# Kernel optimization log

Hardware: AMD Instinct MI355X
Metric: run time of the kernel (lower is better)

Reference implementation:

```python
import jax, jax.numpy as jnp
import numpy as np

K = 3      # spline order
NUM = 5    # grid intervals


def bspline_basis(x, grid, k=K):
    """Cox-de Boor recursion. x: (B, D); grid: (num+2k+1,) extended knots.
    Returns basis of shape (B, D, num+k)."""
    xe = x[..., None]                                       # (B, D, 1)
    B = ((xe >= grid[:-1]) & (xe < grid[1:])).astype(x.dtype)  # (B, D, num+2k)
    for p in range(1, k + 1):
        left = (xe - grid[:-(p + 1)]) / (grid[p:-1] - grid[:-(p + 1)])
        right = (grid[p + 1:] - xe) / (grid[p + 1:] - grid[1:-p])
        B = left * B[..., :-1] + right * B[..., 1:]
    return B                                                # (B, D, num+k)


def kan_layer(x, grid, coef, sb, sp, mask, bias):
    """phi(x)[b,o] = sum_i mask[o,i]*(sb[o,i]*silu(x[b,i]) + sp[o,i]*sum_c B[b,i,c]*coef[o,i,c]) + bias[o]"""
    Bsp = bspline_basis(x, grid)                            # (B, in, C)
    spline = jnp.einsum('bic,oic->bo', Bsp, coef * (sp * mask)[:, :, None])
    base = jnp.einsum('bi,oi->bo', jax.nn.silu(x), sb * mask)
    return base + spline + bias


def setup_inputs() -> dict:
    key = jax.random.key(0)
    ks = jax.random.split(key, 6)
    Bch, d0, d1, d2 = 8192, 1024, 2048, 1024
    C = NUM + K                                 # 8 spline coeffs per edge
    h = 2.0 / NUM                               # grid_range [-1,1]
    # extended knot vector: k extra knots each side, num+2k+1 = 12 points
    grid = jnp.arange(-K, NUM + K + 1, dtype=jnp.float32) * h - 1.0
    return {
        "x": jax.random.normal(ks[0], (Bch, d0), jnp.float32) * 0.5,
        "coef0": jax.random.normal(ks[1], (d1, d0, C), jnp.float32) * 0.1,
        "sb0": jax.random.normal(ks[2], (d1, d0), jnp.float32) / np.sqrt(d0).astype(np.float32),
        "sp0": jnp.ones((d1, d0), jnp.float32),
        "mask0": jnp.ones((d1, d0), jnp.float32),
        "bias0": jnp.zeros((d1,), jnp.float32),
        "coef1": jax.random.normal(ks[3], (d2, d1, C), jnp.float32) * 0.1,
        "sb1": jax.random.normal(ks[4], (d2, d1), jnp.float32) / np.sqrt(d1).astype(np.float32),
        "sp1": jnp.ones((d2, d1), jnp.float32),
        "mask1": jnp.ones((d2, d1), jnp.float32),
        "bias1": jnp.zeros((d2,), jnp.float32),
        "grid": grid,
    }


def reference(x, coef0, sb0, sp0, mask0, bias0, coef1, sb1, sp1, mask1, bias1, grid):
    h1 = kan_layer(x, grid, coef0, sb0, sp0, mask0, bias0)
    out = kan_layer(h1, grid, coef1, sb1, sp1, mask1, bias1)
    return out
```

## Files before the change

### kernel.cpp

```cpp
#include <hip/hip_runtime.h>
#include <hip/hip_bf16.h>
#include <cstdint>


typedef __attribute__((ext_vector_type(8))) short short8;
typedef __attribute__((ext_vector_type(4))) short short4v;
typedef __attribute__((ext_vector_type(4))) float f32x4;

#define GLD16(gp, lp)                                                          \
  __builtin_amdgcn_global_load_lds(                                           \
      (const __attribute__((address_space(1))) unsigned int*)(gp),             \
      (__attribute__((address_space(3))) unsigned int*)(lp), 16, 0, 0)

__device__ __forceinline__ unsigned short f2bf(float f) {
  __hip_bfloat16 h = __float2bfloat16(f);
  return *reinterpret_cast<unsigned short*>(&h);
}

__device__ __forceinline__ void basis8(float x, float* w, int& j) {
  float u  = (x + 2.2f) * 2.5f;
  float fj = floorf(u);
  j = (int)fj;
  float t  = u - fj;
  float omt = 1.0f - t;
  float t2 = t * t, t3 = t2 * t;
  w[0] = omt * omt * omt * (1.0f / 6.0f);
  w[1] = (3.0f * t3 - 6.0f * t2 + 4.0f) * (1.0f / 6.0f);
  w[2] = (-3.0f * t3 + 3.0f * t2 + 3.0f * t + 1.0f) * (1.0f / 6.0f);
  w[3] = t3 * (1.0f / 6.0f);
}

__device__ __forceinline__ void prep_w_item(
    long idx, const float* __restrict__ coef, const float* __restrict__ sb,
    const float* __restrict__ sp, const float* __restrict__ mask,
    __hip_bfloat16* __restrict__ W, int I) {
  int qtr = I >> 2;
  int iq = (int)(idx % qtr);
  int o  = (int)(idx / qtr);
  int i  = iq << 2;
  size_t oi = (size_t)o * I + i;
  float4 mk4 = *(const float4*)(mask + oi);
  float4 sp4 = *(const float4*)(sp + oi);
  float4 sb4 = *(const float4*)(sb + oi);
  float spm[4] = {sp4.x * mk4.x, sp4.y * mk4.y, sp4.z * mk4.z, sp4.w * mk4.w};
  float cf[4][8];
  const float4* cp = (const float4*)(coef + oi * 8);
#pragma unroll
  for (int e = 0; e < 4; e++) {
    float4 a = cp[e * 2], b = cp[e * 2 + 1];
    cf[e][0] = a.x; cf[e][1] = a.y; cf[e][2] = a.z; cf[e][3] = a.w;
    cf[e][4] = b.x; cf[e][5] = b.y; cf[e][6] = b.z; cf[e][7] = b.w;
  }
  __hip_bfloat16* base = W + (size_t)o * (size_t)(9 * I) + (i >> 6) * 576 + (i & 63);
#pragma unroll
  for (int c = 0; c < 8; c++) {
    short4v pk;
#pragma unroll
    for (int e = 0; e < 4; e++) pk[e] = (short)f2bf(cf[e][c] * spm[e]);
    *(short4v*)(base + c * 64) = pk;
  }
  short4v ps;
  ps[0] = (short)f2bf(sb4.x * mk4.x); ps[1] = (short)f2bf(sb4.y * mk4.y);
  ps[2] = (short)f2bf(sb4.z * mk4.z); ps[3] = (short)f2bf(sb4.w * mk4.w);
  *(short4v*)(base + 8 * 64) = ps;
}

__device__ __forceinline__ void expand_item(
    long idx, const float* __restrict__ src, __hip_bfloat16* __restrict__ aug,
    int I) {
  int  oct = I >> 3;
  int  io = (int)(idx % oct);
  long b  = idx / oct;
  int  i  = io << 3;
  const float* sp = src + b * (size_t)I + i;
  float4 xa = *(const float4*)sp;
  float4 xb = *(const float4*)(sp + 4);
  float xv[8] = {xa.x, xa.y, xa.z, xa.w, xb.x, xb.y, xb.z, xb.w};

  float w[8][4], s[8];
  int   j[8];
#pragma unroll
  for (int e = 0; e < 8; e++) {
    float xe = xv[e];
    s[e] = xe / (1.0f + __expf(-xe));
    basis8(xe, w[e], j[e]);
  }
  __hip_bfloat16* base = aug + b * (size_t)(9 * I) + (i >> 6) * 576 + (i & 63);
#pragma unroll
  for (int c = 0; c < 8; c++) {
    short8 pk;
#pragma unroll
    for (int e = 0; e < 8; e++) {
      int d = j[e] - c;
      float v = 0.0f;
      v = (d == 0) ? w[e][3] : v;
      v = (d == 1) ? w[e][2] : v;
      v = (d == 2) ? w[e][1] : v;
      v = (d == 3) ? w[e][0] : v;
      pk[e] = (short)f2bf(v);
    }
    *(short8*)(base + c * 64) = pk;
  }
  short8 ps;
#pragma unroll
  for (int e = 0; e < 8; e++) ps[e] = (short)f2bf(s[e]);
  *(short8*)(base + 8 * 64) = ps;
}

__global__ void prep_merge(
    const float* __restrict__ coef, const float* __restrict__ sb,
    const float* __restrict__ sp, const float* __restrict__ mask,
    __hip_bfloat16* __restrict__ W, int IW, long nW,
    const float* __restrict__ xsrc, __hip_bfloat16* __restrict__ aug,
    int IX, long nX) {
  long idx = (long)blockIdx.x * blockDim.x + threadIdx.x;
  if (idx < nW)            prep_w_item(idx, coef, sb, sp, mask, W, IW);
  else if (idx < nW + nX)  expand_item(idx - nW, xsrc, aug, IX);
}

__global__ void expand_aug(const float* __restrict__ src,
                           __hip_bfloat16* __restrict__ aug,
                           long totalOcts, int I) {
  long idx = (long)blockIdx.x * blockDim.x + threadIdx.x;
  if (idx >= totalOcts) return;
  expand_item(idx, src, aug, I);
}

template <int BN>
__global__ __launch_bounds__(512, 4) void gemm128(
    const __hip_bfloat16* __restrict__ A, const __hip_bfloat16* __restrict__ Bw,
    const float* __restrict__ bias, float* __restrict__ Cout, int N, int K) {
  constexpr int WN   = BN / 4;
  constexpr int NREP = BN / 64;
  constexpr int BUFB = 8192 + BN * 64;
  __shared__ __attribute__((aligned(16))) char lds[3 * BUFB];

  const int t = threadIdx.x;
  const int w = t >> 6, l = t & 63;
  const int wr = w >> 2, wc = w & 3;
  const int lr = l & 15;
  const int kbs = ((l >> 4) * 16) ^ (((lr >> 1) & 3) << 4);

  unsigned nwg = gridDim.x * gridDim.y;
  unsigned lin = blockIdx.y * gridDim.x + blockIdx.x;
  unsigned swz = (lin & 7) * (nwg >> 3) + (lin >> 3);
  unsigned bx = swz % gridDim.x, by = swz / gridDim.x;
  size_t brow = (size_t)by * 128, bcol = (size_t)bx * BN;

  f32x4 acc[4][NREP];
#pragma unroll
  for (int m = 0; m < 4; m++)
#pragma unroll
    for (int n = 0; n < NREP; n++) acc[m][n] = (f32x4){0.f, 0.f, 0.f, 0.f};

  const int srow  = t >> 2;
  const int scolb = ((t & 3) * 16) ^ (((srow >> 1) & 3) << 4);
  const __hip_bfloat16* gA0 = A + (brow + srow) * (size_t)K + (scolb >> 1);
  const __hip_bfloat16* gB0 = Bw + (bcol + srow) * (size_t)K + (scolb >> 1);
  const __hip_bfloat16* gB1 = gB0 + (size_t)128 * K;

  char* ldsp = (char*)lds;
  const int paOff = (wr * 64 + lr) * 64 + kbs;
  const int pbOff = 8192 + (wc * WN + lr) * 64 + kbs;

  auto STAGE = [&](int kt, int q) {
    char* bp = ldsp + q * BUFB;
    GLD16(gA0 + (kt << 5), bp + w * 1024);
    GLD16(gB0 + (kt << 5), bp + 8192 + w * 1024);
    if constexpr (BN == 256) GLD16(gB1 + (kt << 5), bp + 16384 + w * 1024);
  };
  auto COMPUTE = [&](int q) {
    const char* pa = ldsp + q * BUFB + paOff;
    const char* pb = ldsp + q * BUFB + pbOff;
    short8 bq[NREP], aq[4];
#pragma unroll
    for (int n = 0; n < NREP; n++) bq[n] = *(const short8*)(pb + n * 1024);
#pragma unroll
    for (int m = 0; m < 4; m++) aq[m] = *(const short8*)(pa + m * 1024);
    __builtin_amdgcn_s_setprio(1);
#pragma unroll
    for (int m = 0; m < 4; m++)
#pragma unroll
      for (int n = 0; n < NREP; n++)
        acc[m][n] = __builtin_amdgcn_mfma_f32_16x16x32_bf16(aq[m], bq[n], acc[m][n], 0, 0, 0);
    __builtin_amdgcn_s_setprio(0);
    __builtin_amdgcn_s_barrier();
  };
  auto VM0 = [&]() { asm volatile("s_waitcnt vmcnt(0)" ::: "memory"); };
  auto VML = [&]() {
    if constexpr (BN == 256) asm volatile("s_waitcnt vmcnt(3)" ::: "memory");
    else                     asm volatile("s_waitcnt vmcnt(2)" ::: "memory");
  };
  auto VM2L = [&]() {
    if constexpr (BN == 256) asm volatile("s_waitcnt vmcnt(6)" ::: "memory");
    else                     asm volatile("s_waitcnt vmcnt(4)" ::: "memory");
  };

  const int NT = K >> 5;

  STAGE(0, 0);
  STAGE(1, 1);
  VML();
  __builtin_amdgcn_s_barrier();

  int q0 = 0;
  for (int kt = 0; kt < NT - 2; ++kt) {
    int q2 = q0 + 2; if (q2 >= 3) q2 -= 3;
    STAGE(kt + 2, q2);
    VM2L();
    __builtin_amdgcn_s_barrier();
    COMPUTE(q0);
    q0 = (q0 == 2) ? 0 : q0 + 1;
  }
  VML();
  __builtin_amdgcn_s_barrier();
  COMPUTE(q0);
  q0 = (q0 == 2) ? 0 : q0 + 1;
  VM0();
  __builtin_amdgcn_s_barrier();
  COMPUTE(q0);

  const int orow = (l >> 4) << 2;
#pragma unroll
  for (int n = 0; n < NREP; n++) {
    size_t col = bcol + (size_t)wc * WN + n * 16 + lr;
    float bv = bias[col];
#pragma unroll
    for (int m = 0; m < 4; m++) {
      size_t row = brow + (size_t)wr * 64 + m * 16 + orow;
#pragma unroll
      for (int r = 0; r < 4; r++)
        Cout[(row + r) * (size_t)N + col] = acc[m][n][r] + bv;
    }
  }
}

__global__ __launch_bounds__(512, 4) void gemm64n(
    const __hip_bfloat16* __restrict__ A, const __hip_bfloat16* __restrict__ Bw,
    const float* __restrict__ bias, float* __restrict__ Cout, int N, int K) {
  constexpr int BUFB = 8192 + 4096;
  __shared__ __attribute__((aligned(16))) char lds[3 * BUFB];

  const int t = threadIdx.x;
  const int w = t >> 6, l = t & 63;
  const int wr = w >> 2, wc = w & 3;
  const int lr = l & 15;
  const int kbs = ((l >> 4) * 16) ^ (((lr >> 1) & 3) << 4);

  unsigned nwg = gridDim.x * gridDim.y;
  unsigned lin = blockIdx.y * gridDim.x + blockIdx.x;
  unsigned swz = (lin & 7) * (nwg >> 3) + (lin >> 3);
  unsigned bx = swz % gridDim.x, by = swz / gridDim.x;
  size_t brow = (size_t)by * 128, bcol = (size_t)bx * 64;

  f32x4 acc[4];
#pragma unroll
  for (int m = 0; m < 4; m++) acc[m] = (f32x4){0.f, 0.f, 0.f, 0.f};

  const int srow  = t >> 2;
  const int scolb = ((t & 3) * 16) ^ (((srow >> 1) & 3) << 4);
  const __hip_bfloat16* gA0 = A + (brow + srow) * (size_t)K + (scolb >> 1);
  const int tb  = t & 255;
  const int srB = tb >> 2;
  const int scB = ((tb & 3) * 16) ^ (((srB >> 1) & 3) << 4);
  const __hip_bfloat16* gB0 = Bw + (bcol + srB) * (size_t)K + (scB >> 1);

  char* ldsp = (char*)lds;
  const int paOff = (wr * 64 + lr) * 64 + kbs;
  const int pbOff = 8192 + (wc * 16 + lr) * 64 + kbs;

  auto STAGE = [&](int kt, int q) {
    char* bp = ldsp + q * BUFB;
    GLD16(gA0 + (kt << 5), bp + w * 1024);
    GLD16(gB0 + (kt << 5), bp + 8192 + (w & 3) * 1024);
  };
  auto COMPUTE = [&](int q) {
    const char* pa = ldsp + q * BUFB + paOff;
    const char* pb = ldsp + q * BUFB + pbOff;
    short8 bq = *(const short8*)pb;
    short8 aq[4];
#pragma unroll
    for (int m = 0; m < 4; m++) aq[m] = *(const short8*)(pa + m * 1024);
    __builtin_amdgcn_s_setprio(1);
#pragma unroll
    for (int m = 0; m < 4; m++)
      acc[m] = __builtin_amdgcn_mfma_f32_16x16x32_bf16(aq[m], bq, acc[m], 0, 0, 0);
    __builtin_amdgcn_s_setprio(0);
    __builtin_amdgcn_s_barrier();
  };

  const int NT = K >> 5;

  STAGE(0, 0);
  STAGE(1, 1);
  asm volatile("s_waitcnt vmcnt(2)" ::: "memory");
  __builtin_amdgcn_s_barrier();

  int q0 = 0;
  for (int kt = 0; kt < NT - 2; ++kt) {
    int q2 = q0 + 2; if (q2 >= 3) q2 -= 3;
    STAGE(kt + 2, q2);
    asm volatile("s_waitcnt vmcnt(4)" ::: "memory");
    __builtin_amdgcn_s_barrier();
    COMPUTE(q0);
    q0 = (q0 == 2) ? 0 : q0 + 1;
  }
  asm volatile("s_waitcnt vmcnt(2)" ::: "memory");
  __builtin_amdgcn_s_barrier();
  COMPUTE(q0);
  q0 = (q0 == 2) ? 0 : q0 + 1;
  asm volatile("s_waitcnt vmcnt(0)" ::: "memory");
  __builtin_amdgcn_s_barrier();
  COMPUTE(q0);

  const int orow = (l >> 4) << 2;
  size_t col = bcol + (size_t)wc * 16 + lr;
  float bv = bias[col];
#pragma unroll
  for (int m = 0; m < 4; m++) {
    size_t row = brow + (size_t)wr * 64 + m * 16 + orow;
#pragma unroll
    for (int r = 0; r < 4; r++)
      Cout[(row + r) * (size_t)N + col] = acc[m][r] + bv;
  }
}

extern "C" void kernel_launch(void* const* d_in, const int* in_sizes, int n_in,
                              void* d_out, int out_size, void* d_ws, size_t ws_size,
                              hipStream_t stream) {
  const float* x     = (const float*)d_in[0];
  const float* coef0 = (const float*)d_in[1];
  const float* sb0   = (const float*)d_in[2];
  const float* sp0   = (const float*)d_in[3];
  const float* mask0 = (const float*)d_in[4];
  const float* bias0 = (const float*)d_in[5];
  const float* coef1 = (const float*)d_in[6];
  const float* sb1   = (const float*)d_in[7];
  const float* sp1   = (const float*)d_in[8];
  const float* mask1 = (const float*)d_in[9];
  const float* bias1 = (const float*)d_in[10];
  float* out = (float*)d_out;

  const int B = 8192, D0 = 1024, D1 = 2048, D2 = 1024;
  const int K0 = 9 * D0;
  const int K1 = 9 * D1;
  const int CH = 4096;

  char* ws = (char*)d_ws;
  float*          h1  = (float*)ws;
  __hip_bfloat16* W   = (__hip_bfloat16*)(ws + (size_t)67108864);
  __hip_bfloat16* Aug = (__hip_bfloat16*)(ws + (size_t)104857600);

  const long nW0 = (long)D1 * (D0 / 4);
  const long nX0 = (long)B * (D0 / 8);
  const long nW1 = (long)D2 * (D1 / 4);
  const long nX1 = (long)CH * (D1 / 8);

  prep_merge<<<(unsigned)((nW0 + nX0) / 256), 256, 0, stream>>>(
      coef0, sb0, sp0, mask0, W, D0, nW0, x, Aug, D0, nX0);
  {
    dim3 g0(D1 / 256, B / 128);
    gemm128<256><<<g0, 512, 0, stream>>>(Aug, W, bias0, h1, D1, K0);
  }

  prep_merge<<<(unsigned)((nW1 + nX1) / 256), 256, 0, stream>>>(
      coef1, sb1, sp1, mask1, W, D1, nW1, h1, Aug, D1, nX1);
  {
    dim3 g1(D2 / 64, CH / 128);
    gemm64n<<<g1, 512, 0, stream>>>(Aug, W, bias1, out, D2, K1);
  }
  expand_aug<<<(unsigned)(nX1 / 256), 256, 0, stream>>>(
      h1 + (size_t)CH * D1, Aug, nX1, D1);
  {
    dim3 g1(D2 / 64, CH / 128);
    gemm64n<<<g1, 512, 0, stream>>>(Aug, W, bias1,
                                    out + (size_t)CH * D2, D2, K1);
  }
}
```

Measured before the change: 955.9 us.

## Use 128x128 split-K tiles for second-layer GEMM with partial-sum reduction

Replaces the 128x64 tile GEMM for layer two with a 128x128 tile kernel that splits K in two. This keeps the block count the same while doubling per-tile data reuse. The second K-half writes partials to a scratch buffer that reuses already-consumed h1 workspace. A separate elementwise kernel then adds them into the output. This trades extra global traffic and launch overhead for higher arithmetic intensity per block.

```diff
diff --git a/kernel.cpp b/kernel.cpp
--- a/kernel.cpp
+++ b/kernel.cpp
@@ -126,6 +126,16 @@
   expand_item(idx, src, aug, I);
 }
 
+__global__ void reduce_add(float* __restrict__ out, const float* __restrict__ part,
+                           long n4) {
+  long i = (long)blockIdx.x * blockDim.x + threadIdx.x;
+  if (i >= n4) return;
+  float4 a = *(const float4*)(out + i * 4);
+  float4 b = *(const float4*)(part + i * 4);
+  a.x += b.x; a.y += b.y; a.z += b.z; a.w += b.w;
+  *(float4*)(out + i * 4) = a;
+}
+
 template <int BN>
 __global__ __launch_bounds__(512, 4) void gemm128(
     const __hip_bfloat16* __restrict__ A, const __hip_bfloat16* __restrict__ Bw,
@@ -235,10 +245,11 @@
   }
 }
 
-__global__ __launch_bounds__(512, 4) void gemm64n(
+__global__ __launch_bounds__(512, 4) void gemm128s(
     const __hip_bfloat16* __restrict__ A, const __hip_bfloat16* __restrict__ Bw,
-    const float* __restrict__ bias, float* __restrict__ Cout, int N, int K) {
-  constexpr int BUFB = 8192 + 4096;
+    const float* __restrict__ bias, float* __restrict__ Cout,
+    float* __restrict__ Part, int N, int K, int KS) {
+  constexpr int BUFB = 8192 + 8192;
   __shared__ __attribute__((aligned(16))) char lds[3 * BUFB];
 
   const int t = threadIdx.x;
@@ -250,46 +261,50 @@
   unsigned nwg = gridDim.x * gridDim.y;
   unsigned lin = blockIdx.y * gridDim.x + blockIdx.x;
   unsigned swz = (lin & 7) * (nwg >> 3) + (lin >> 3);
-  unsigned bx = swz % gridDim.x, by = swz / gridDim.x;
-  size_t brow = (size_t)by * 128, bcol = (size_t)bx * 64;
-
-  f32x4 acc[4];
-#pragma unroll
-  for (int m = 0; m < 4; m++) acc[m] = (f32x4){0.f, 0.f, 0.f, 0.f};
+  unsigned bx = swz % gridDim.x, byf = swz / gridDim.x;
+  const int kz = (int)(byf >> 5);
+  size_t brow = (size_t)(byf & 31) * 128, bcol = (size_t)bx * 128;
+  const int kofs = kz * KS;
+
+  f32x4 acc[4][2];
+#pragma unroll
+  for (int m = 0; m < 4; m++)
+#pragma unroll
+    for (int n = 0; n < 2; n++) acc[m][n] = (f32x4){0.f, 0.f, 0.f, 0.f};
 
   const int srow  = t >> 2;
   const int scolb = ((t & 3) * 16) ^ (((srow >> 1) & 3) << 4);
-  const __hip_bfloat16* gA0 = A + (brow + srow) * (size_t)K + (scolb >> 1);
-  const int tb  = t & 255;
-  const int srB = tb >> 2;
-  const int scB = ((tb & 3) * 16) ^ (((srB >> 1) & 3) << 4);
-  const __hip_bfloat16* gB0 = Bw + (bcol + srB) * (size_t)K + (scB >> 1);
+  const __hip_bfloat16* gA0 = A + (brow + srow) * (size_t)K + kofs + (scolb >> 1);
+  const __hip_bfloat16* gB0 = Bw + (bcol + srow) * (size_t)K + kofs + (scolb >> 1);
 
   char* ldsp = (char*)lds;
   const int paOff = (wr * 64 + lr) * 64 + kbs;
-  const int pbOff = 8192 + (wc * 16 + lr) * 64 + kbs;
+  const int pbOff = 8192 + (wc * 32 + lr) * 64 + kbs;
 
   auto STAGE = [&](int kt, int q) {
     char* bp = ldsp + q * BUFB;
     GLD16(gA0 + (kt << 5), bp + w * 1024);
-    GLD16(gB0 + (kt << 5), bp + 8192 + (w & 3) * 1024);
+    GLD16(gB0 + (kt << 5), bp + 8192 + w * 1024);
   };
   auto COMPUTE = [&](int q) {
     const char* pa = ldsp + q * BUFB + paOff;
     const char* pb = ldsp + q * BUFB + pbOff;
-    short8 bq = *(const short8*)pb;
-    short8 aq[4];
+    short8 bq[2], aq[4];
+#pragma unroll
+    for (int n = 0; n < 2; n++) bq[n] = *(const short8*)(pb + n * 1024);
 #pragma unroll
     for (int m = 0; m < 4; m++) aq[m] = *(const short8*)(pa + m * 1024);
     __builtin_amdgcn_s_setprio(1);
 #pragma unroll
     for (int m = 0; m < 4; m++)
-      acc[m] = __builtin_amdgcn_mfma_f32_16x16x32_bf16(aq[m], bq, acc[m], 0, 0, 0);
+#pragma unroll
+      for (int n = 0; n < 2; n++)
+        acc[m][n] = __builtin_amdgcn_mfma_f32_16x16x32_bf16(aq[m], bq[n], acc[m][n], 0, 0, 0);
     __builtin_amdgcn_s_setprio(0);
     __builtin_amdgcn_s_barrier();
   };
 
-  const int NT = K >> 5;
+  const int NT = KS >> 5;
 
   STAGE(0, 0);
   STAGE(1, 1);
@@ -314,14 +329,18 @@
   COMPUTE(q0);
 
   const int orow = (l >> 4) << 2;
-  size_t col = bcol + (size_t)wc * 16 + lr;
-  float bv = bias[col];
-#pragma unroll
-  for (int m = 0; m < 4; m++) {
-    size_t row = brow + (size_t)wr * 64 + m * 16 + orow;
-#pragma unroll
-    for (int r = 0; r < 4; r++)
-      Cout[(row + r) * (size_t)N + col] = acc[m][r] + bv;
+  float* C = (kz == 0) ? Cout : Part;
+#pragma unroll
+  for (int n = 0; n < 2; n++) {
+    size_t col = bcol + (size_t)wc * 32 + n * 16 + lr;
+    float bv = (kz == 0) ? bias[col] : 0.0f;
+#pragma unroll
+    for (int m = 0; m < 4; m++) {
+      size_t row = brow + (size_t)wr * 64 + m * 16 + orow;
+#pragma unroll
+      for (int r = 0; r < 4; r++)
+        C[(row + r) * (size_t)N + col] = acc[m][n][r] + bv;
+    }
   }
 }
 
@@ -350,11 +369,14 @@
   float*          h1  = (float*)ws;
   __hip_bfloat16* W   = (__hip_bfloat16*)(ws + (size_t)67108864);
   __hip_bfloat16* Aug = (__hip_bfloat16*)(ws + (size_t)104857600);
+  float* P0 = (float*)ws;
+  float* P1 = (float*)(ws + (size_t)33554432);
 
   const long nW0 = (long)D1 * (D0 / 4);
   const long nX0 = (long)B * (D0 / 8);
   const long nW1 = (long)D2 * (D1 / 4);
   const long nX1 = (long)CH * (D1 / 8);
+  const long n4  = (long)CH * D2 / 4;
 
   prep_merge<<<(unsigned)((nW0 + nX0) / 256), 256, 0, stream>>>(
       coef0, sb0, sp0, mask0, W, D0, nW0, x, Aug, D0, nX0);
@@ -366,14 +388,17 @@
   prep_merge<<<(unsigned)((nW1 + nX1) / 256), 256, 0, stream>>>(
       coef1, sb1, sp1, mask1, W, D1, nW1, h1, Aug, D1, nX1);
   {
-    dim3 g1(D2 / 64, CH / 128);
-    gemm64n<<<g1, 512, 0, stream>>>(Aug, W, bias1, out, D2, K1);
-  }
+    dim3 g1(D2 / 128, 2 * CH / 128);
+    gemm128s<<<g1, 512, 0, stream>>>(Aug, W, bias1, out, P0, D2, K1, K1 / 2);
+    reduce_add<<<(unsigned)(n4 / 256), 256, 0, stream>>>(out, P0, n4);
+  }
+
   expand_aug<<<(unsigned)(nX1 / 256), 256, 0, stream>>>(
       h1 + (size_t)CH * D1, Aug, nX1, D1);
   {
-    dim3 g1(D2 / 64, CH / 128);
-    gemm64n<<<g1, 512, 0, stream>>>(Aug, W, bias1,
-                                    out + (size_t)CH * D2, D2, K1);
-  }
-}
+    dim3 g1(D2 / 128, 2 * CH / 128);
+    gemm128s<<<g1, 512, 0, stream>>>(Aug, W, bias1, out + (size_t)CH * D2,
+                                     P1, D2, K1, K1 / 2);
+    reduce_add<<<(unsigned)(n4 / 256), 256, 0, stream>>>(out + (size_t)CH * D2, P1, n4);
+  }
+}
```

Measured after the change: 802.7 us. 16.0% less time.
